# Performance work log

Hardware: AMD Instinct MI355X
Metric: run time of the kernel (lower is better)

## Reference

```python
import jax, jax.numpy as jnp
import numpy as np

N, C, H, W = 32, 128, 64, 64
D_BOT, K = 512, 7
EPS = 1e-5


def setup_inputs() -> dict:
    key = jax.random.key(0)
    ks = jax.random.split(key, 4)
    init = lambda k, shape, fan: (jax.random.normal(k, shape, jnp.float32) / np.sqrt(fan).astype(np.float32))
    return {
        "x": jax.random.normal(ks[0], (N, C, H, W), jnp.float32),
        "dw_w": init(ks[1], (C, 1, K, K), K * K),          # depthwise kernel, OIHW with I=1
        "dw_b": jnp.zeros((C,), jnp.float32),
        "gamma": jnp.ones((C,), jnp.float32),
        "beta": jnp.zeros((C,), jnp.float32),
        "pw1_w": init(ks[2], (D_BOT, C), C),               # 1x1 conv == channel matmul
        "pw1_b": jnp.zeros((D_BOT,), jnp.float32),
        "pw2_w": init(ks[3], (C, D_BOT), D_BOT),
        "pw2_b": jnp.zeros((C,), jnp.float32),
    }


def reference(x, dw_w, dw_b, gamma, beta, pw1_w, pw1_b, pw2_w, pw2_b):
    # depthwise 7x7 conv, stride 1, 'same' padding (NCHW)
    y = jax.lax.conv_general_dilated(
        x, dw_w, window_strides=(1, 1), padding="SAME",
        dimension_numbers=("NCHW", "OIHW", "NCHW"),
        feature_group_count=x.shape[1],
    ) + dw_b[None, :, None, None]
    # NCHW -> NHWC for channel LayerNorm
    y = jnp.transpose(y, (0, 2, 3, 1))
    mu = jnp.mean(y, axis=-1, keepdims=True)
    var = jnp.mean(jnp.square(y - mu), axis=-1, keepdims=True)
    y = (y - mu) * jax.lax.rsqrt(var + EPS) * gamma + beta
    # pointwise MLP: 1x1 convs are channel-mixing matmuls
    h = jax.nn.relu(jnp.einsum("nhwc,dc->nhwd", y, pw1_w) + pw1_b)
    o = jnp.einsum("nhwd,cd->nhwc", h, pw2_w) + pw2_b
    # back to NCHW + residual
    return x + jnp.transpose(o, (0, 3, 1, 2))
```

## Files before the change

### kernel.cpp

```cpp
#include <hip/hip_runtime.h>
#include <hip/hip_bf16.h>

#define NB   32
#define CCH  128
#define HH   64
#define WW   64
#define DBOT 512
#define EPS_LN 1e-5f

typedef __attribute__((ext_vector_type(8))) short bf16x8;
typedef __attribute__((ext_vector_type(4))) float f32x4;

__global__ __launch_bounds__(256) void wcvt_kernel(
    const float* __restrict__ w1, const float* __restrict__ w2,
    __hip_bfloat16* __restrict__ o1, __hip_bfloat16* __restrict__ o2)
{
    int i = blockIdx.x * 256 + threadIdx.x;
    o1[i] = __float2bfloat16(w1[i]);
    o2[i] = __float2bfloat16(w2[i]);
}

#define XS 76

__global__ __launch_bounds__(256) void dwconv_kernel(
    const float* __restrict__ x, const float* __restrict__ dw_w,
    const float* __restrict__ dw_b, __hip_bfloat16* __restrict__ cout)
{
    __shared__ float xs[64 * XS];

    const int t = threadIdx.x;
    const int n = blockIdx.x >> 7;
    const int c = blockIdx.x & 127;

    const float* xp = x + ((size_t)(n * CCH + c) << 12);

    #pragma unroll
    for (int i = 0; i < 4; ++i) {
        int idx = i * 256 + t;
        int r   = idx >> 4;
        int c4  = idx & 15;
        float4 v = ((const float4*)xp)[idx];
        *(float4*)&xs[r * XS + 4 + c4 * 4] = v;
    }
    #pragma unroll
    for (int i = 0; i < 3; ++i) {
        int idx = i * 256 + t;
        int r   = idx / 12;
        int p   = idx % 12;
        int col = (p < 4) ? p : (p + 64);
        xs[r * XS + col] = 0.0f;
    }

    float wgt[49];
    const float* wp = dw_w + c * 49;
    #pragma unroll
    for (int j = 0; j < 49; ++j) wgt[j] = wp[j];
    const float bias = dw_b[c];

    __syncthreads();

    const int h  = t >> 2;
    const int w0 = (t & 3) << 4;

    float acc[16];
    #pragma unroll
    for (int j = 0; j < 16; ++j) acc[j] = bias;

    #pragma unroll
    for (int kh = 0; kh < 7; ++kh) {
        int hh = h + kh - 3;
        if (hh < 0 || hh >= HH) continue;
        float r[24];
        const float* row = &xs[hh * XS + w0];
        #pragma unroll
        for (int j = 0; j < 6; ++j) *(float4*)&r[j * 4] = *(const float4*)&row[j * 4];
        #pragma unroll
        for (int kw = 0; kw < 7; ++kw)
            #pragma unroll
            for (int j = 0; j < 16; ++j)
                acc[j] = fmaf(r[j + kw + 1], wgt[kh * 7 + kw], acc[j]);
    }

    union { uint4 q[2]; __hip_bfloat16 b[16]; } pk;
    #pragma unroll
    for (int j = 0; j < 16; ++j) pk.b[j] = __float2bfloat16(acc[j]);
    __hip_bfloat16* op = cout + (((size_t)(n * CCH + c)) << 12) + (h << 6) + w0;
    *(uint4*)op       = pk.q[0];
    *(uint4*)(op + 8) = pk.q[1];
}

#define YS 136
#define OS 65

__global__ __launch_bounds__(256) void mlp_kernel(
    const __hip_bfloat16* __restrict__ conv,
    const float* __restrict__ gamma,
    const float* __restrict__ beta,
    const __hip_bfloat16* __restrict__ w1,
    const float* __restrict__ b1,
    const __hip_bfloat16* __restrict__ w2,
    const float* __restrict__ b2,
    const float* __restrict__ x,
    float* __restrict__ out)
{
    __shared__ union {
        struct { unsigned short y[64 * YS]; unsigned short h[64 * YS]; } s;
        float o[CCH * OS];
    } u;
    __shared__ float sPart[2][4 * 64];
    __shared__ float sMu[64], sRstd[64];

    const int t    = threadIdx.x;
    const int wave = t >> 6;
    const int lane = t & 63;
    const int q    = lane >> 4;
    const int ln   = lane & 15;
    const int wm   = (wave >> 1) * 32;
    const int wn   = (wave & 1) * 64;

    const int n = blockIdx.x >> 6;
    const int h = blockIdx.x & 63;

    {
        const int wI = t & 63;
        const int cg = t >> 6;
        const __hip_bfloat16* crow = conv + ((size_t)n << 19) + (h << 6);
        float vals[32];
        float s = 0.f, s2 = 0.f;
        #pragma unroll
        for (int j = 0; j < 32; ++j) {
            int c = cg * 32 + j;
            float v = __bfloat162float(crow[((size_t)c << 12) + wI]);
            vals[j] = v;
            s += v;
            s2 = fmaf(v, v, s2);
        }
        sPart[0][cg * 64 + wI] = s;
        sPart[1][cg * 64 + wI] = s2;
        __syncthreads();
        if (t < 64) {
            float su = 0.f, sq = 0.f;
            #pragma unroll
            for (int g = 0; g < 4; ++g) { su += sPart[0][g * 64 + t]; sq += sPart[1][g * 64 + t]; }
            float mu  = su * (1.0f / 128.0f);
            float var = sq * (1.0f / 128.0f) - mu * mu;
            sMu[t]   = mu;
            sRstd[t] = 1.0f / sqrtf(var + EPS_LN);
        }
        __syncthreads();
        float mu = sMu[wI], rs = sRstd[wI];
        #pragma unroll
        for (int j = 0; j < 32; ++j) {
            int c = cg * 32 + j;
            float r = (vals[j] - mu) * rs * gamma[c] + beta[c];
            __hip_bfloat16 hb = __float2bfloat16(r);
            u.s.y[wI * YS + c] = *(unsigned short*)&hb;
        }
    }

    f32x4 oacc[2][4];
    #pragma unroll
    for (int mt = 0; mt < 2; ++mt)
        #pragma unroll
        for (int ct = 0; ct < 4; ++ct) oacc[mt][ct] = (f32x4){0.f, 0.f, 0.f, 0.f};

    __syncthreads();

    for (int dc = 0; dc < 4; ++dc) {
        const int d0 = dc * 128;
        f32x4 hacc[2][4];
        #pragma unroll
        for (int mt = 0; mt < 2; ++mt)
            #pragma unroll
            for (int dt = 0; dt < 4; ++dt) hacc[mt][dt] = (f32x4){0.f, 0.f, 0.f, 0.f};

        #pragma unroll
        for (int k0 = 0; k0 < 128; k0 += 32) {
            bf16x8 af[2];
            #pragma unroll
            for (int mt = 0; mt < 2; ++mt)
                af[mt] = *(const bf16x8*)&u.s.y[(wm + mt * 16 + ln) * YS + k0 + q * 8];
            bf16x8 bw[4];
            #pragma unroll
            for (int dt = 0; dt < 4; ++dt) {
                int d = d0 + wn + dt * 16 + ln;
                bw[dt] = *(const bf16x8*)(w1 + (size_t)d * 128 + k0 + q * 8);
            }
            #pragma unroll
            for (int mt = 0; mt < 2; ++mt)
                #pragma unroll
                for (int dt = 0; dt < 4; ++dt)
                    hacc[mt][dt] = __builtin_amdgcn_mfma_f32_16x16x32_bf16(
                        af[mt], bw[dt], hacc[mt][dt], 0, 0, 0);
        }

        __syncthreads();

        #pragma unroll
        for (int mt = 0; mt < 2; ++mt) {
            #pragma unroll
            for (int dt = 0; dt < 4; ++dt) {
                int dl = wn + dt * 16 + ln;
                float bv = b1[d0 + dl];
                #pragma unroll
                for (int r = 0; r < 4; ++r) {
                    float v = hacc[mt][dt][r] + bv;
                    v = fmaxf(v, 0.0f);
                    __hip_bfloat16 hb = __float2bfloat16(v);
                    u.s.h[(wm + mt * 16 + q * 4 + r) * YS + dl] = *(unsigned short*)&hb;
                }
            }
        }
        __syncthreads();

        #pragma unroll
        for (int k0 = 0; k0 < 128; k0 += 32) {
            bf16x8 af[2];
            #pragma unroll
            for (int mt = 0; mt < 2; ++mt)
                af[mt] = *(const bf16x8*)&u.s.h[(wm + mt * 16 + ln) * YS + k0 + q * 8];
            bf16x8 bw[4];
            #pragma unroll
            for (int ct = 0; ct < 4; ++ct) {
                int c = wn + ct * 16 + ln;
                bw[ct] = *(const bf16x8*)(w2 + (size_t)c * DBOT + d0 + k0 + q * 8);
            }
            #pragma unroll
            for (int mt = 0; mt < 2; ++mt)
                #pragma unroll
                for (int ct = 0; ct < 4; ++ct)
                    oacc[mt][ct] = __builtin_amdgcn_mfma_f32_16x16x32_bf16(
                        af[mt], bw[ct], oacc[mt][ct], 0, 0, 0);
        }
    }

    __syncthreads();

    #pragma unroll
    for (int mt = 0; mt < 2; ++mt) {
        #pragma unroll
        for (int ct = 0; ct < 4; ++ct) {
            int c = wn + ct * 16 + ln;
            #pragma unroll
            for (int r = 0; r < 4; ++r)
                u.o[c * OS + wm + mt * 16 + q * 4 + r] = oacc[mt][ct][r];
        }
    }
    __syncthreads();

    const float* xb = x   + ((size_t)(n * CCH) << 12) + (h << 6);
    float*       ob = out + ((size_t)(n * CCH) << 12) + (h << 6);
    for (int i = 0; i < 32; ++i) {
        int linear = i * 256 + t;
        int c  = linear >> 6;
        int wi = linear & 63;
        float v = u.o[c * OS + wi] + b2[c] + xb[(size_t)c * 4096 + wi];
        ob[(size_t)c * 4096 + wi] = v;
    }
}

extern "C" void kernel_launch(void* const* d_in, const int* in_sizes, int n_in,
                              void* d_out, int out_size, void* d_ws, size_t ws_size,
                              hipStream_t stream)
{
    const float* x     = (const float*)d_in[0];
    const float* dw_w  = (const float*)d_in[1];
    const float* dw_b  = (const float*)d_in[2];
    const float* gamma = (const float*)d_in[3];
    const float* beta  = (const float*)d_in[4];
    const float* pw1_w = (const float*)d_in[5];
    const float* pw1_b = (const float*)d_in[6];
    const float* pw2_w = (const float*)d_in[7];
    const float* pw2_b = (const float*)d_in[8];
    float* out = (float*)d_out;

    char* ws = (char*)d_ws;
    __hip_bfloat16* convb = (__hip_bfloat16*)ws;
    __hip_bfloat16* w1b   = (__hip_bfloat16*)(ws + (size_t)33554432);
    __hip_bfloat16* w2b   = (__hip_bfloat16*)(ws + (size_t)33554432 + 131072);

    wcvt_kernel<<<256, 256, 0, stream>>>(pw1_w, pw2_w, w1b, w2b);
    dwconv_kernel<<<NB * CCH, 256, 0, stream>>>(x, dw_w, dw_b, convb);
    mlp_kernel<<<NB * HH, 256, 0, stream>>>(convb, gamma, beta, w1b, pw1_b, w2b, pw2_b, x, out);
}
```

Before: 296.1 us.

## Store conv output as per-row NHCW tiles and keep LN activations in registers

The depthwise conv now writes its bf16 output in an (n,h,c,w) layout, so each MLP block reads one contiguous 16KB tile with vectorized loads instead of 128 strided channel rows. The LayerNorm result is built directly into MFMA A-fragments held in registers, which drops the LDS y buffer and a barrier. The epilogue writes output with float4 stores straight from the accumulators, removing the LDS transpose stage. Launch bounds now request 4 blocks per CU, which may raise register pressure from the extra fragment registers.

```diff
diff --git a/kernel.cpp b/kernel.cpp
--- a/kernel.cpp
+++ b/kernel.cpp
@@ -10,6 +10,14 @@
 
 typedef __attribute__((ext_vector_type(8))) short bf16x8;
 typedef __attribute__((ext_vector_type(4))) float f32x4;
+
+__device__ __forceinline__ float bf2f(unsigned short u) {
+    return __uint_as_float(((unsigned)u) << 16);
+}
+__device__ __forceinline__ unsigned short f2bf(float f) {
+    __hip_bfloat16 h = __float2bfloat16(f);
+    return *(unsigned short*)&h;
+}
 
 __global__ __launch_bounds__(256) void wcvt_kernel(
     const float* __restrict__ w1, const float* __restrict__ w2,
@@ -24,7 +32,7 @@
 
 __global__ __launch_bounds__(256) void dwconv_kernel(
     const float* __restrict__ x, const float* __restrict__ dw_w,
-    const float* __restrict__ dw_b, __hip_bfloat16* __restrict__ cout)
+    const float* __restrict__ dw_b, unsigned short* __restrict__ cout)
 {
     __shared__ float xs[64 * XS];
 
@@ -81,19 +89,30 @@
                 acc[j] = fmaf(r[j + kw + 1], wgt[kh * 7 + kw], acc[j]);
     }
 
-    union { uint4 q[2]; __hip_bfloat16 b[16]; } pk;
-    #pragma unroll
-    for (int j = 0; j < 16; ++j) pk.b[j] = __float2bfloat16(acc[j]);
-    __hip_bfloat16* op = cout + (((size_t)(n * CCH + c)) << 12) + (h << 6) + w0;
-    *(uint4*)op       = pk.q[0];
-    *(uint4*)(op + 8) = pk.q[1];
-}
-
-#define YS 136
-#define OS 65
-
-__global__ __launch_bounds__(256) void mlp_kernel(
-    const __hip_bfloat16* __restrict__ conv,
+    uint4 s0, s1;
+    {
+        __hip_bfloat162 p0 = __float22bfloat162_rn(make_float2(acc[0],  acc[1]));
+        __hip_bfloat162 p1 = __float22bfloat162_rn(make_float2(acc[2],  acc[3]));
+        __hip_bfloat162 p2 = __float22bfloat162_rn(make_float2(acc[4],  acc[5]));
+        __hip_bfloat162 p3 = __float22bfloat162_rn(make_float2(acc[6],  acc[7]));
+        __hip_bfloat162 p4 = __float22bfloat162_rn(make_float2(acc[8],  acc[9]));
+        __hip_bfloat162 p5 = __float22bfloat162_rn(make_float2(acc[10], acc[11]));
+        __hip_bfloat162 p6 = __float22bfloat162_rn(make_float2(acc[12], acc[13]));
+        __hip_bfloat162 p7 = __float22bfloat162_rn(make_float2(acc[14], acc[15]));
+        s0.x = *(unsigned*)&p0; s0.y = *(unsigned*)&p1;
+        s0.z = *(unsigned*)&p2; s0.w = *(unsigned*)&p3;
+        s1.x = *(unsigned*)&p4; s1.y = *(unsigned*)&p5;
+        s1.z = *(unsigned*)&p6; s1.w = *(unsigned*)&p7;
+    }
+    unsigned short* op = cout + ((size_t)((n * 64 + h) * 128 + c) << 6) + w0;
+    *(uint4*)op       = s0;
+    *(uint4*)(op + 8) = s1;
+}
+
+#define HS 136
+
+__global__ __launch_bounds__(256, 4) void mlp_kernel(
+    const unsigned short* __restrict__ conv,
     const float* __restrict__ gamma,
     const float* __restrict__ beta,
     const __hip_bfloat16* __restrict__ w1,
@@ -104,10 +123,10 @@
     float* __restrict__ out)
 {
     __shared__ union {
-        struct { unsigned short y[64 * YS]; unsigned short h[64 * YS]; } s;
-        float o[CCH * OS];
+        unsigned short xs[CCH * 64];
+        unsigned short h[64 * HS];
     } u;
-    __shared__ float sPart[2][4 * 64];
+    __shared__ float sPart[2][256];
     __shared__ float sMu[64], sRstd[64];
 
     const int t    = threadIdx.x;
@@ -122,39 +141,62 @@
     const int h = blockIdx.x & 63;
 
     {
-        const int wI = t & 63;
-        const int cg = t >> 6;
-        const __hip_bfloat16* crow = conv + ((size_t)n << 19) + (h << 6);
-        float vals[32];
+        const uint4* src = (const uint4*)(conv + ((size_t)blockIdx.x << 13));
+        #pragma unroll
+        for (int i = 0; i < 4; ++i) {
+            int idx = i * 256 + t;
+            uint4 v = src[idx];
+            *(uint4*)&u.xs[idx * 8] = v;
+        }
+    }
+    __syncthreads();
+
+    {
+        const int wI = t & 63, cg = t >> 6;
         float s = 0.f, s2 = 0.f;
         #pragma unroll
         for (int j = 0; j < 32; ++j) {
-            int c = cg * 32 + j;
-            float v = __bfloat162float(crow[((size_t)c << 12) + wI]);
-            vals[j] = v;
+            float v = bf2f(u.xs[(cg * 32 + j) * 64 + wI]);
             s += v;
             s2 = fmaf(v, v, s2);
         }
         sPart[0][cg * 64 + wI] = s;
         sPart[1][cg * 64 + wI] = s2;
-        __syncthreads();
-        if (t < 64) {
-            float su = 0.f, sq = 0.f;
-            #pragma unroll
-            for (int g = 0; g < 4; ++g) { su += sPart[0][g * 64 + t]; sq += sPart[1][g * 64 + t]; }
-            float mu  = su * (1.0f / 128.0f);
-            float var = sq * (1.0f / 128.0f) - mu * mu;
-            sMu[t]   = mu;
-            sRstd[t] = 1.0f / sqrtf(var + EPS_LN);
-        }
-        __syncthreads();
-        float mu = sMu[wI], rs = sRstd[wI];
-        #pragma unroll
-        for (int j = 0; j < 32; ++j) {
-            int c = cg * 32 + j;
-            float r = (vals[j] - mu) * rs * gamma[c] + beta[c];
-            __hip_bfloat16 hb = __float2bfloat16(r);
-            u.s.y[wI * YS + c] = *(unsigned short*)&hb;
+    }
+    __syncthreads();
+    if (t < 64) {
+        float su = 0.f, sq = 0.f;
+        #pragma unroll
+        for (int g = 0; g < 4; ++g) { su += sPart[0][g * 64 + t]; sq += sPart[1][g * 64 + t]; }
+        float mu  = su * (1.0f / 128.0f);
+        float var = sq * (1.0f / 128.0f) - mu * mu;
+        sMu[t]   = mu;
+        sRstd[t] = 1.0f / sqrtf(var + EPS_LN);
+    }
+    __syncthreads();
+
+    bf16x8 af[2][4];
+    #pragma unroll
+    for (int mt = 0; mt < 2; ++mt) {
+        const int pos = wm + mt * 16 + ln;
+        const float mu = sMu[pos], rs = sRstd[pos];
+        #pragma unroll
+        for (int kb = 0; kb < 4; ++kb) {
+            const int c0 = kb * 32 + q * 8;
+            float4 g0  = *(const float4*)(gamma + c0);
+            float4 g1  = *(const float4*)(gamma + c0 + 4);
+            float4 be0 = *(const float4*)(beta + c0);
+            float4 be1 = *(const float4*)(beta + c0 + 4);
+            float gv[8] = {g0.x, g0.y, g0.z, g0.w, g1.x, g1.y, g1.z, g1.w};
+            float bv[8] = {be0.x, be0.y, be0.z, be0.w, be1.x, be1.y, be1.z, be1.w};
+            bf16x8 a;
+            #pragma unroll
+            for (int j = 0; j < 8; ++j) {
+                float v = bf2f(u.xs[(c0 + j) * 64 + pos]);
+                float r = (v - mu) * rs * gv[j] + bv[j];
+                a[j] = (short)f2bf(r);
+            }
+            af[mt][kb] = a;
         }
     }
 
@@ -163,11 +205,10 @@
     for (int mt = 0; mt < 2; ++mt)
         #pragma unroll
         for (int ct = 0; ct < 4; ++ct) oacc[mt][ct] = (f32x4){0.f, 0.f, 0.f, 0.f};
-
-    __syncthreads();
 
     for (int dc = 0; dc < 4; ++dc) {
         const int d0 = dc * 128;
+
         f32x4 hacc[2][4];
         #pragma unroll
         for (int mt = 0; mt < 2; ++mt)
@@ -175,87 +216,74 @@
             for (int dt = 0; dt < 4; ++dt) hacc[mt][dt] = (f32x4){0.f, 0.f, 0.f, 0.f};
 
         #pragma unroll
-        for (int k0 = 0; k0 < 128; k0 += 32) {
-            bf16x8 af[2];
-            #pragma unroll
-            for (int mt = 0; mt < 2; ++mt)
-                af[mt] = *(const bf16x8*)&u.s.y[(wm + mt * 16 + ln) * YS + k0 + q * 8];
+        for (int kb = 0; kb < 4; ++kb) {
             bf16x8 bw[4];
             #pragma unroll
             for (int dt = 0; dt < 4; ++dt) {
                 int d = d0 + wn + dt * 16 + ln;
-                bw[dt] = *(const bf16x8*)(w1 + (size_t)d * 128 + k0 + q * 8);
+                bw[dt] = *(const bf16x8*)(w1 + (size_t)d * 128 + kb * 32 + q * 8);
             }
             #pragma unroll
             for (int mt = 0; mt < 2; ++mt)
                 #pragma unroll
                 for (int dt = 0; dt < 4; ++dt)
                     hacc[mt][dt] = __builtin_amdgcn_mfma_f32_16x16x32_bf16(
-                        af[mt], bw[dt], hacc[mt][dt], 0, 0, 0);
+                        af[mt][kb], bw[dt], hacc[mt][dt], 0, 0, 0);
         }
 
         __syncthreads();
 
         #pragma unroll
-        for (int mt = 0; mt < 2; ++mt) {
-            #pragma unroll
-            for (int dt = 0; dt < 4; ++dt) {
-                int dl = wn + dt * 16 + ln;
-                float bv = b1[d0 + dl];
+        for (int dt = 0; dt < 4; ++dt) {
+            const int dl = wn + dt * 16 + ln;
+            const float b1v = b1[d0 + dl];
+            #pragma unroll
+            for (int mt = 0; mt < 2; ++mt) {
                 #pragma unroll
                 for (int r = 0; r < 4; ++r) {
-                    float v = hacc[mt][dt][r] + bv;
-                    v = fmaxf(v, 0.0f);
-                    __hip_bfloat16 hb = __float2bfloat16(v);
-                    u.s.h[(wm + mt * 16 + q * 4 + r) * YS + dl] = *(unsigned short*)&hb;
+                    float v = fmaxf(hacc[mt][dt][r] + b1v, 0.0f);
+                    u.h[(wm + mt * 16 + q * 4 + r) * HS + dl] = f2bf(v);
                 }
             }
         }
         __syncthreads();
 
         #pragma unroll
-        for (int k0 = 0; k0 < 128; k0 += 32) {
-            bf16x8 af[2];
+        for (int kb = 0; kb < 4; ++kb) {
+            bf16x8 ah[2];
             #pragma unroll
             for (int mt = 0; mt < 2; ++mt)
-                af[mt] = *(const bf16x8*)&u.s.h[(wm + mt * 16 + ln) * YS + k0 + q * 8];
-            bf16x8 bw[4];
+                ah[mt] = *(const bf16x8*)&u.h[(wm + mt * 16 + ln) * HS + kb * 32 + q * 8];
+            bf16x8 bw2[4];
             #pragma unroll
             for (int ct = 0; ct < 4; ++ct) {
                 int c = wn + ct * 16 + ln;
-                bw[ct] = *(const bf16x8*)(w2 + (size_t)c * DBOT + d0 + k0 + q * 8);
+                bw2[ct] = *(const bf16x8*)(w2 + (size_t)c * DBOT + d0 + kb * 32 + q * 8);
             }
             #pragma unroll
             for (int mt = 0; mt < 2; ++mt)
                 #pragma unroll
                 for (int ct = 0; ct < 4; ++ct)
                     oacc[mt][ct] = __builtin_amdgcn_mfma_f32_16x16x32_bf16(
-                        af[mt], bw[ct], oacc[mt][ct], 0, 0, 0);
-        }
-    }
-
-    __syncthreads();
-
-    #pragma unroll
-    for (int mt = 0; mt < 2; ++mt) {
-        #pragma unroll
-        for (int ct = 0; ct < 4; ++ct) {
-            int c = wn + ct * 16 + ln;
-            #pragma unroll
-            for (int r = 0; r < 4; ++r)
-                u.o[c * OS + wm + mt * 16 + q * 4 + r] = oacc[mt][ct][r];
-        }
-    }
-    __syncthreads();
-
-    const float* xb = x   + ((size_t)(n * CCH) << 12) + (h << 6);
-    float*       ob = out + ((size_t)(n * CCH) << 12) + (h << 6);
-    for (int i = 0; i < 32; ++i) {
-        int linear = i * 256 + t;
-        int c  = linear >> 6;
-        int wi = linear & 63;
-        float v = u.o[c * OS + wi] + b2[c] + xb[(size_t)c * 4096 + wi];
-        ob[(size_t)c * 4096 + wi] = v;
+                        ah[mt], bw2[ct], oacc[mt][ct], 0, 0, 0);
+        }
+    }
+
+    #pragma unroll
+    for (int ct = 0; ct < 4; ++ct) {
+        const int c = wn + ct * 16 + ln;
+        const float b2v = b2[c];
+        #pragma unroll
+        for (int mt = 0; mt < 2; ++mt) {
+            size_t base = ((size_t)(n * CCH + c) << 12) + (h << 6) + wm + mt * 16 + q * 4;
+            float4 xr = *(const float4*)(x + base);
+            float4 o;
+            o.x = oacc[mt][ct][0] + b2v + xr.x;
+            o.y = oacc[mt][ct][1] + b2v + xr.y;
+            o.z = oacc[mt][ct][2] + b2v + xr.z;
+            o.w = oacc[mt][ct][3] + b2v + xr.w;
+            *(float4*)(out + base) = o;
+        }
     }
 }
 
@@ -275,7 +303,7 @@
     float* out = (float*)d_out;
 
     char* ws = (char*)d_ws;
-    __hip_bfloat16* convb = (__hip_bfloat16*)ws;
+    unsigned short* convb = (unsigned short*)ws;
     __hip_bfloat16* w1b   = (__hip_bfloat16*)(ws + (size_t)33554432);
     __hip_bfloat16* w2b   = (__hip_bfloat16*)(ws + (size_t)33554432 + 131072);
 
```

Measured after the change: 284.7 us. 3.8% less time.
